# Performance work log

Measured on AMD Instinct MI355X. Metric: run time of the kernel, lower is better.

## Reference

```python
import jax, jax.numpy as jnp
import numpy as np

NUM_LEAVES = 8192
N_LAMBDA = 2101  # wavelengths 400..2500 nm

# ---- exponential integral E1(x), x > 0 (Abramowitz & Stegun 5.1.53 / 5.1.56) ----
# Ei(-x) = -E1(x) for x > 0; forward only ever calls expi on -kall with kall >= 1e-4.
_A = jnp.array([-0.57721566, 0.99999193, -0.24991055, 0.05519968, -0.00976004, 0.00107857], dtype=jnp.float32)
_PN = jnp.array([1.0, 8.5733287401, 18.0590169730, 8.6347608925, 0.2677737343], dtype=jnp.float32)
_PD = jnp.array([1.0, 9.5733223454, 25.6329561486, 21.0996530827, 3.9584969228], dtype=jnp.float32)

def _poly(c, x):
    r = c[0]
    for ci in c[1:]:
        r = r * x + ci
    return r

def _e1(x):
    # x > 0 guaranteed (kall clamped to >= 1e-4)
    small = -jnp.log(x) + _poly(_A[::-1], x)          # 0 < x <= 1
    big = jnp.exp(-x) / x * (_poly(_PN, x) / _poly(_PD, x))  # x > 1
    return jnp.where(x <= 1.0, small, big)

# ---- transmissivity of a dielectric plane (Stern / Allen) ----
def _getav(alpha_deg, nr):
    n2 = nr ** 2
    npx = n2 + 1.0
    nm = n2 - 1.0
    a = (nr + 1.0) * (nr + 1.0) / 2.0
    k = -(n2 - 1.0) * (n2 - 1.0) / 4.0
    rd = alpha_deg * (np.pi / 180.0)
    sa2 = np.sin(rd) ** 2  # python scalar
    if alpha_deg != 90.0:
        b1 = jnp.sqrt((sa2 - npx / 2.0) ** 2 + k)
    else:
        b1 = 0.0
    b2 = sa2 - npx / 2.0
    b = b1 - b2
    k2 = k ** 2
    ts = k2 / (6.0 * b ** 3) + k / b - b / 2.0 - (k2 / (6.0 * a ** 3) + k / a - a / 2.0)
    tp1 = -2.0 * n2 * (b - a) / npx ** 2
    nm2 = nm ** 2
    tp2 = -2.0 * n2 * npx * jnp.log(b / a) / nm2
    tp3 = n2 * (1.0 / b - 1.0 / a) / 2.0
    n22 = n2 ** 2
    npx3 = npx ** 3
    npax_a = 2.0 * npx * a - nm2
    npx_b = 2.0 * npx * b - nm2
    tp4 = 16.0 * n22 * (n22 + 1.0) * jnp.log(npx_b / npax_a) / (npx3 * nm2)
    tp5 = 16.0 * n2 ** 3 * (1.0 / npx_b - 1.0 / npax_a) / npx3
    tp = tp1 + tp2 + tp3 + tp4 + tp5
    return (ts + tp) / (2.0 * sa2)

def _forward(N, cab, car, water, lma, cant, nr, kab, kcar, kant, kw, km):
    # kall: [L, W] via broadcasting of [L,1] traits against [W] spectra
    kall = (cab * kab + car * kcar + cant * kant + water * kw + lma * km) / N
    kall = jnp.maximum(kall, 1e-4)
    # tau = (1-k)e^{-k} + k^2 * (-Ei(-k)) = (1-k)e^{-k} + k^2 E1(k)
    tau = (1.0 - kall) * jnp.exp(-kall) + kall ** 2 * _e1(kall)

    # one-layer reflectance/transmittance
    talf = _getav(40.0, nr)
    ralf = 1.0 - talf
    t12 = _getav(90.0, nr)
    r12 = 1.0 - t12
    t21 = t12 / (nr * nr)
    r21 = 1.0 - t21
    denom = 1.0 - r21 * r21 * tau * tau
    Ta = talf * tau * t21 / denom
    Ra = ralf + r21 * tau * Ta
    t = t12 * tau * t21 / denom
    r = r12 + r21 * tau * t

    rpt = r + t
    rmt = r - t
    mask = rpt >= 1.0  # [L, W]
    Dsq = (1.0 + rpt) * (1.0 + rmt) * (1.0 - rmt) * (1.0 - rpt)
    D = jnp.sqrt(jnp.where(mask, 1.0, Dsq))
    rqmtq = r ** 2 - t ** 2
    a = (1.0 + rqmtq + D) / (2.0 * r)
    b = (1.0 - rqmtq + D) / (2.0 * t)
    b_safe = jnp.where(mask, 1.0, b)  # guard pow with float exponent
    bnm1 = b_safe ** (N - 1.0)
    bn2 = bnm1 ** 2
    a2 = a * a
    den2 = a2 * bn2 - 1.0
    Rsub = a * (bn2 - 1.0) / den2
    Tsub = bnm1 * (a2 - 1.0) / den2
    # thick-layer (r+t >= 1) limit
    Tsub_alt = t / (t + (1.0 - t) * (N - 1.0))
    Tsub = jnp.where(mask, Tsub_alt, Tsub)
    Rsub = jnp.where(mask, 1.0 - Tsub_alt, Rsub)

    den3 = 1.0 - Rsub * r
    tran = Ta * Tsub / den3
    refl = Ra + Ta_Rsub_term(Ta, Rsub, t, den3)
    return refl, tran

def Ta_Rsub_term(Ta, Rsub, t, den3):
    return Ta * Rsub * t / den3

def setup_inputs() -> dict:
    key = jax.random.key(0)
    ks = jax.random.split(key, 12)
    u = lambda k, shp: jax.random.uniform(k, shp, dtype=jnp.float32)
    L, W = NUM_LEAVES, N_LAMBDA
    return {
        "N":     1.0 + 1.5 * u(ks[0], (L, 1)),      # leaf structure 1..2.5
        "cab":   10.0 + 70.0 * u(ks[1], (L, 1)),    # chlorophyll ug/cm2
        "car":   2.0 + 18.0 * u(ks[2], (L, 1)),     # carotenoids
        "water": 0.002 + 0.03 * u(ks[3], (L, 1)),   # EWT cm
        "lma":   0.005 + 0.03 * u(ks[4], (L, 1)),   # dry matter g/cm2
        "cant":  2.0 * u(ks[5], (L, 1)),            # anthocyanins
        "nr":    1.3 + 0.3 * u(ks[6], (W,)),        # refractive index
        "kab":   0.05 * u(ks[7], (W,)),
        "kcar":  0.05 * u(ks[8], (W,)),
        "kant":  0.05 * u(ks[9], (W,)),
        "kw":    30.0 * u(ks[10], (W,)),
        "km":    60.0 * u(ks[11], (W,)),
    }

def reference(N, cab, car, water, lma, cant, nr, kab, kcar, kant, kw, km):
    return _forward(N, cab, car, water, lma, cant, nr, kab, kcar, kant, kw, km)
```

## Files before the change

kernel.cpp:

```cpp
#include <hip/hip_runtime.h>

#define L_LEAVES 8192
#define W_LAMBDA 2101
#define WPAD     2104
#define NL       8
#define SA2_40   0.41317591116653485f
#define LOG2E_F  1.4426950408889634f
#define LN2_F    0.6931471805599453f

__device__ __forceinline__ float rcpf(float x)  { return __builtin_amdgcn_rcpf(x); }
__device__ __forceinline__ float log2f_fast(float x) { return __builtin_amdgcn_logf(x); }
__device__ __forceinline__ float exp2f_fast(float x) { return __builtin_amdgcn_exp2f(x); }
__device__ __forceinline__ float sqrtf_fast(float x) { return __builtin_amdgcn_sqrtf(x); }

__device__ __forceinline__ float getav_dev(float sa2, bool is90, float nr) {
    float n2  = nr * nr;
    float npx = n2 + 1.0f;
    float nm  = n2 - 1.0f;
    float a   = (nr + 1.0f) * (nr + 1.0f) * 0.5f;
    float k   = -(n2 - 1.0f) * (n2 - 1.0f) * 0.25f;
    float b2  = sa2 - npx * 0.5f;
    float b1  = is90 ? 0.0f : sqrtf(b2 * b2 + k);
    float b   = b1 - b2;
    float k2  = k * k;
    float b3  = b * b * b;
    float a3  = a * a * a;
    float ts  = k2 / (6.0f * b3) + k / b - b * 0.5f
              - (k2 / (6.0f * a3) + k / a - a * 0.5f);
    float tp1 = -2.0f * n2 * (b - a) / (npx * npx);
    float nm2 = nm * nm;
    float tp2 = -2.0f * n2 * npx * logf(b / a) / nm2;
    float tp3 = n2 * (1.0f / b - 1.0f / a) * 0.5f;
    float n22 = n2 * n2;
    float npx3 = npx * npx * npx;
    float npax_a = 2.0f * npx * a - nm2;
    float npx_b  = 2.0f * npx * b - nm2;
    float tp4 = 16.0f * n22 * (n22 + 1.0f) * logf(npx_b / npax_a) / (npx3 * nm2);
    float tp5 = 16.0f * n2 * n2 * n2 * (1.0f / npx_b - 1.0f / npax_a) / npx3;
    float tp  = tp1 + tp2 + tp3 + tp4 + tp5;
    return (ts + tp) / (2.0f * sa2);
}

__global__ void precompute_kernel(const float* __restrict__ nr, float* __restrict__ tab) {
    int w = blockIdx.x * blockDim.x + threadIdx.x;
    if (w >= W_LAMBDA) return;
    float n    = nr[w];
    float talf = getav_dev(SA2_40, false, n);
    float t12  = getav_dev(1.0f,   true,  n);
    float t21  = t12 * rcpf(n * n);
    float r21  = 1.0f - t21;
    tab[0 * WPAD + w] = talf * t21;
    tab[1 * WPAD + w] = 1.0f - talf;
    tab[2 * WPAD + w] = t12 * t21;
    tab[3 * WPAD + w] = 1.0f - t12;
    tab[4 * WPAD + w] = r21;
    tab[5 * WPAD + w] = r21 * r21;
}

struct f4u { float v[4]; };

__device__ __forceinline__ float vget(const float4& v, int j) {
    return j == 0 ? v.x : (j == 1 ? v.y : (j == 2 ? v.z : v.w));
}

template<bool USE_TAB>
__global__ __launch_bounds__(64) void prospect_kernel(
    const float* __restrict__ pN,   const float* __restrict__ pcab,
    const float* __restrict__ pcar, const float* __restrict__ pwater,
    const float* __restrict__ plma, const float* __restrict__ pcant,
    const float* __restrict__ pnr,
    const float* __restrict__ pkab, const float* __restrict__ pkcar,
    const float* __restrict__ pkant, const float* __restrict__ pkw,
    const float* __restrict__ pkm,
    const float* __restrict__ tab,
    float* __restrict__ out)
{
    const int q  = blockIdx.x * 64 + threadIdx.x;
    const int w0 = q * 4;
    if (w0 >= W_LAMBDA) return;
    const bool full = (w0 + 4 <= W_LAMBDA);
    const int l0 = blockIdx.y * NL;
    const size_t LW = (size_t)L_LEAVES * W_LAMBDA;

    float4 vkab, vkcar, vkant, vkw, vkm;
    float4 t0, t1, t2, t3, t4, t5;
    if (full) {
        vkab  = *(const float4*)(pkab  + w0);
        vkcar = *(const float4*)(pkcar + w0);
        vkant = *(const float4*)(pkant + w0);
        vkw   = *(const float4*)(pkw   + w0);
        vkm   = *(const float4*)(pkm   + w0);
    } else {
        #pragma unroll
        for (int j = 0; j < 4; ++j) {
            int w = min(w0 + j, W_LAMBDA - 1);
            ((float*)&vkab)[j]  = pkab[w];
            ((float*)&vkcar)[j] = pkcar[w];
            ((float*)&vkant)[j] = pkant[w];
            ((float*)&vkw)[j]   = pkw[w];
            ((float*)&vkm)[j]   = pkm[w];
        }
    }
    if (USE_TAB) {
        if (full) {
            t0 = *(const float4*)(tab + 0 * WPAD + w0);
            t1 = *(const float4*)(tab + 1 * WPAD + w0);
            t2 = *(const float4*)(tab + 2 * WPAD + w0);
            t3 = *(const float4*)(tab + 3 * WPAD + w0);
            t4 = *(const float4*)(tab + 4 * WPAD + w0);
            t5 = *(const float4*)(tab + 5 * WPAD + w0);
        } else {
            #pragma unroll
            for (int j = 0; j < 4; ++j) {
                int w = min(w0 + j, W_LAMBDA - 1);
                ((float*)&t0)[j] = tab[0 * WPAD + w];
                ((float*)&t1)[j] = tab[1 * WPAD + w];
                ((float*)&t2)[j] = tab[2 * WPAD + w];
                ((float*)&t3)[j] = tab[3 * WPAD + w];
                ((float*)&t4)[j] = tab[4 * WPAD + w];
                ((float*)&t5)[j] = tab[5 * WPAD + w];
            }
        }
    } else {
        #pragma unroll
        for (int j = 0; j < 4; ++j) {
            int w = min(w0 + j, W_LAMBDA - 1);
            float n    = pnr[w];
            float talf = getav_dev(SA2_40, false, n);
            float t12  = getav_dev(1.0f,   true,  n);
            float t21  = t12 * rcpf(n * n);
            float r21  = 1.0f - t21;
            ((float*)&t0)[j] = talf * t21;
            ((float*)&t1)[j] = 1.0f - talf;
            ((float*)&t2)[j] = t12 * t21;
            ((float*)&t3)[j] = 1.0f - t12;
            ((float*)&t4)[j] = r21;
            ((float*)&t5)[j] = r21 * r21;
        }
    }

    #pragma unroll 1
    for (int il = 0; il < NL; ++il) {
        const int l = l0 + il;
        const float Nl   = pN[l];
        const float invN = rcpf(Nl);
        const float Nm1  = Nl - 1.0f;
        const float cabl = pcab[l], carl = pcar[l], cantl = pcant[l];
        const float watl = pwater[l], lmal = plma[l];

        float rf[4], tr[4];
        #pragma unroll
        for (int j = 0; j < 4; ++j) {
            const float c0 = vget(t0, j), c1 = vget(t1, j), c2 = vget(t2, j);
            const float c3 = vget(t3, j), c4 = vget(t4, j), c5 = vget(t5, j);

            float k = (cabl * vget(vkab, j) + carl * vget(vkcar, j) + cantl * vget(vkant, j)
                     + watl * vget(vkw, j) + lmal * vget(vkm, j)) * invN;
            k = fmaxf(k, 1e-4f);

            float ek   = exp2f_fast(-k * LOG2E_F);
            float lg2k = log2f_fast(k);
            float poly = fmaf(fmaf(fmaf(fmaf(fmaf(0.00107857f, k, -0.00976004f), k, 0.05519968f),
                            k, -0.24991055f), k, 0.99999193f), k, -0.57721566f);
            float e1s  = fmaf(-LN2_F, lg2k, poly);
            float taus = fmaf(k * k, e1s, (1.0f - k) * ek);
            float pn = fmaf(fmaf(fmaf(fmaf(1.0f, k, 8.5733287401f), k, 18.0590169730f),
                           k, 8.6347608925f), k, 0.2677737343f);
            float pd = fmaf(fmaf(fmaf(fmaf(1.0f, k, 9.5733223454f), k, 25.6329561486f),
                           k, 21.0996530827f), k, 3.9584969228f);
            float taub = ek * fmaf(k, pn - pd, pd) * rcpf(pd);
            float tau  = (k <= 1.0f) ? taus : taub;

            float tau2 = tau * tau;
            float rd   = rcpf(fmaf(-c5, tau2, 1.0f));
            float Ta   = c0 * tau * rd;
            float tt   = c2 * tau * rd;
            float r21t = c4 * tau;
            float Ra   = fmaf(r21t, Ta, c1);
            float rr   = fmaf(r21t, tt, c3);

            float rpt  = rr + tt;
            float rmt  = rr - tt;
            bool  mask = (rpt >= 1.0f);
            float Dsq  = fmaf(-rmt, rmt, 1.0f) * fmaf(-rpt, rpt, 1.0f);
            float D    = sqrtf_fast(mask ? 1.0f : Dsq);
            float rq   = rpt * rmt;
            float s1   = 1.0f + D;
            float rp2  = rcpf((rr * tt) * 4.0f);
            float aa   = (s1 + rq) * (rp2 * (tt + tt));
            float bb   = (s1 - rq) * (rp2 * (rr + rr));
            float bsafe = mask ? 1.0f : bb;
            float bnm1 = exp2f_fast(Nm1 * log2f_fast(bsafe));
            float bn2  = bnm1 * bnm1;
            float a2   = aa * aa;
            float rdn  = rcpf(fmaf(a2, bn2, -1.0f));
            float Rsub = aa * (bn2 - 1.0f) * rdn;
            float Tsub = bnm1 * (a2 - 1.0f) * rdn;
            if (__any((int)mask)) {
                float Talt = tt * rcpf(fmaf(Nm1, 1.0f - tt, tt));
                if (mask) { Tsub = Talt; Rsub = 1.0f - Talt; }
            }

            float r3   = rcpf(fmaf(-Rsub, rr, 1.0f));
            float g    = Ta * r3;
            tr[j] = g * Tsub;
            rf[j] = fmaf(g * Rsub, tt, Ra);
        }

        const size_t base = (size_t)l * W_LAMBDA + w0;
        if (full) {
            f4u fr; f4u ft;
            #pragma unroll
            for (int j = 0; j < 4; ++j) { fr.v[j] = rf[j]; ft.v[j] = tr[j]; }
            *reinterpret_cast<f4u*>(out + base)      = fr;
            *reinterpret_cast<f4u*>(out + LW + base) = ft;
        } else {
            out[base]      = rf[0];
            out[LW + base] = tr[0];
        }
    }
}

extern "C" void kernel_launch(void* const* d_in, const int* in_sizes, int n_in,
                              void* d_out, int out_size, void* d_ws, size_t ws_size,
                              hipStream_t stream) {
    const float* pN     = (const float*)d_in[0];
    const float* pcab   = (const float*)d_in[1];
    const float* pcar   = (const float*)d_in[2];
    const float* pwater = (const float*)d_in[3];
    const float* plma   = (const float*)d_in[4];
    const float* pcant  = (const float*)d_in[5];
    const float* pnr    = (const float*)d_in[6];
    const float* pkab   = (const float*)d_in[7];
    const float* pkcar  = (const float*)d_in[8];
    const float* pkant  = (const float*)d_in[9];
    const float* pkw    = (const float*)d_in[10];
    const float* pkm    = (const float*)d_in[11];
    float* out = (float*)d_out;

    const int nquads = (W_LAMBDA + 3) / 4;
    dim3 grid((nquads + 63) / 64, L_LEAVES / NL);
    dim3 block(64);

    const size_t tab_bytes = 6 * WPAD * sizeof(float);
    if (ws_size >= tab_bytes) {
        float* tabp = (float*)d_ws;
        precompute_kernel<<<(W_LAMBDA + 255) / 256, 256, 0, stream>>>(pnr, tabp);
        prospect_kernel<true><<<grid, block, 0, stream>>>(
            pN, pcab, pcar, pwater, plma, pcant, pnr,
            pkab, pkcar, pkant, pkw, pkm, (const float*)tabp, out);
    } else {
        prospect_kernel<false><<<grid, block, 0, stream>>>(
            pN, pcab, pcar, pwater, plma, pcant, pnr,
            pkab, pkcar, pkant, pkw, pkm, nullptr, out);
    }
}
```

Baseline: 64.09 us.

## Assign one leaf per block row and merge substrate division algebra

Drops the per-thread loop over 8 leaves, so each block now handles a single leaf with 192 threads across wavelengths, and the grid grows to 8192 rows. The substrate and top-layer combination is rewritten algebraically so a single reciprocal replaces two. The aim is more parallelism and latency hiding, plus fewer transcendental ops per element. In exchange every thread reloads the per-wavelength spectra and table values for each leaf instead of reusing them across 8 leaves, which adds load traffic and many more blocks. It also wastes threads in the last column of blocks (526 quads spread over 3 blocks of 192).

```diff
diff --git a/kernel.cpp b/kernel.cpp
--- a/kernel.cpp
+++ b/kernel.cpp
@@ -3,7 +3,6 @@
 #define L_LEAVES 8192
 #define W_LAMBDA 2101
 #define WPAD     2104
-#define NL       8
 #define SA2_40   0.41317591116653485f
 #define LOG2E_F  1.4426950408889634f
 #define LN2_F    0.6931471805599453f
@@ -64,7 +63,7 @@
 }
 
 template<bool USE_TAB>
-__global__ __launch_bounds__(64) void prospect_kernel(
+__global__ __launch_bounds__(192) void prospect_kernel(
     const float* __restrict__ pN,   const float* __restrict__ pcab,
     const float* __restrict__ pcar, const float* __restrict__ pwater,
     const float* __restrict__ plma, const float* __restrict__ pcant,
@@ -75,11 +74,17 @@
     const float* __restrict__ tab,
     float* __restrict__ out)
 {
-    const int q  = blockIdx.x * 64 + threadIdx.x;
+    const int q  = blockIdx.x * blockDim.x + threadIdx.x;
     const int w0 = q * 4;
     if (w0 >= W_LAMBDA) return;
     const bool full = (w0 + 4 <= W_LAMBDA);
-    const int l0 = blockIdx.y * NL;
+
+    const int l = blockIdx.y;
+    const float Nl   = pN[l];
+    const float invN = rcpf(Nl);
+    const float Nm1  = Nl - 1.0f;
+    const float cabl = pcab[l], carl = pcar[l], cantl = pcant[l];
+    const float watl = pwater[l], lmal = plma[l];
     const size_t LW = (size_t)L_LEAVES * W_LAMBDA;
 
     float4 vkab, vkcar, vkant, vkw, vkm;
@@ -139,85 +144,82 @@
         }
     }
 
-    #pragma unroll 1
-    for (int il = 0; il < NL; ++il) {
-        const int l = l0 + il;
-        const float Nl   = pN[l];
-        const float invN = rcpf(Nl);
-        const float Nm1  = Nl - 1.0f;
-        const float cabl = pcab[l], carl = pcar[l], cantl = pcant[l];
-        const float watl = pwater[l], lmal = plma[l];
-
-        float rf[4], tr[4];
+    float rf[4], tr[4];
+    #pragma unroll
+    for (int j = 0; j < 4; ++j) {
+        const float c0 = vget(t0, j), c1 = vget(t1, j), c2 = vget(t2, j);
+        const float c3 = vget(t3, j), c4 = vget(t4, j), c5 = vget(t5, j);
+
+        float k = (cabl * vget(vkab, j) + carl * vget(vkcar, j) + cantl * vget(vkant, j)
+                 + watl * vget(vkw, j) + lmal * vget(vkm, j)) * invN;
+        k = fmaxf(k, 1e-4f);
+
+        float ek   = exp2f_fast(-k * LOG2E_F);
+        float lg2k = log2f_fast(k);
+        float poly = fmaf(fmaf(fmaf(fmaf(fmaf(0.00107857f, k, -0.00976004f), k, 0.05519968f),
+                        k, -0.24991055f), k, 0.99999193f), k, -0.57721566f);
+        float e1s  = fmaf(-LN2_F, lg2k, poly);
+        float taus = fmaf(k * k, e1s, fmaf(-k, ek, ek));
+        float pn = fmaf(fmaf(fmaf(k + 8.5733287401f, k, 18.0590169730f),
+                       k, 8.6347608925f), k, 0.2677737343f);
+        float pd = fmaf(fmaf(fmaf(k + 9.5733223454f, k, 25.6329561486f),
+                       k, 21.0996530827f), k, 3.9584969228f);
+        float taub = ek * fmaf(k, pn - pd, pd) * rcpf(pd);
+        float tau  = (k <= 1.0f) ? taus : taub;
+
+        float tau2 = tau * tau;
+        float rd   = rcpf(fmaf(-c5, tau2, 1.0f));
+        float trd  = tau * rd;
+        float Ta   = c0 * trd;
+        float tt   = c2 * trd;
+        float r21t = c4 * tau;
+        float Ra   = fmaf(r21t, Ta, c1);
+        float rr   = fmaf(r21t, tt, c3);
+
+        float rpt  = rr + tt;
+        float rmt  = rr - tt;
+        bool  mask = (rpt >= 1.0f);
+        float Dsq  = fmaf(-rmt, rmt, 1.0f) * fmaf(-rpt, rpt, 1.0f);
+        float D    = sqrtf_fast(mask ? 1.0f : Dsq);
+        float rq   = rpt * rmt;
+        float s1   = 1.0f + D;
+        float rp2  = rcpf((rr * tt) * 4.0f);
+        float aa   = (s1 + rq) * (rp2 * (tt + tt));
+        float bb   = (s1 - rq) * (rp2 * (rr + rr));
+        float bsafe = mask ? 1.0f : bb;
+        float bnm1 = exp2f_fast(Nm1 * log2f_fast(bsafe));
+        float bn2  = bnm1 * bnm1;
+        float a2   = aa * aa;
+        float den2 = fmaf(a2, bn2, -1.0f);
+        float bn2m1 = bn2 - 1.0f;
+        float aarr  = aa * rr;
+        float M     = fmaf(-aarr, bn2m1, den2);
+        float invM  = rcpf(M);
+        float TaM   = Ta * invM;
+        float tranj = TaM * bnm1 * (a2 - 1.0f);
+        float reflj = fmaf(TaM * tt * aa, bn2m1, Ra);
+
+        if (__any((int)mask)) {
+            float Talt = tt * rcpf(fmaf(Nm1, 1.0f - tt, tt));
+            float Rsm  = 1.0f - Talt;
+            float g    = Ta * rcpf(fmaf(-Rsm, rr, 1.0f));
+            if (mask) { tranj = g * Talt; reflj = fmaf(g * Rsm, tt, Ra); }
+        }
+
+        tr[j] = tranj;
+        rf[j] = reflj;
+    }
+
+    const size_t base = (size_t)l * W_LAMBDA + w0;
+    if (full) {
+        f4u fr; f4u ft;
         #pragma unroll
-        for (int j = 0; j < 4; ++j) {
-            const float c0 = vget(t0, j), c1 = vget(t1, j), c2 = vget(t2, j);
-            const float c3 = vget(t3, j), c4 = vget(t4, j), c5 = vget(t5, j);
-
-            float k = (cabl * vget(vkab, j) + carl * vget(vkcar, j) + cantl * vget(vkant, j)
-                     + watl * vget(vkw, j) + lmal * vget(vkm, j)) * invN;
-            k = fmaxf(k, 1e-4f);
-
-            float ek   = exp2f_fast(-k * LOG2E_F);
-            float lg2k = log2f_fast(k);
-            float poly = fmaf(fmaf(fmaf(fmaf(fmaf(0.00107857f, k, -0.00976004f), k, 0.05519968f),
-                            k, -0.24991055f), k, 0.99999193f), k, -0.57721566f);
-            float e1s  = fmaf(-LN2_F, lg2k, poly);
-            float taus = fmaf(k * k, e1s, (1.0f - k) * ek);
-            float pn = fmaf(fmaf(fmaf(fmaf(1.0f, k, 8.5733287401f), k, 18.0590169730f),
-                           k, 8.6347608925f), k, 0.2677737343f);
-            float pd = fmaf(fmaf(fmaf(fmaf(1.0f, k, 9.5733223454f), k, 25.6329561486f),
-                           k, 21.0996530827f), k, 3.9584969228f);
-            float taub = ek * fmaf(k, pn - pd, pd) * rcpf(pd);
-            float tau  = (k <= 1.0f) ? taus : taub;
-
-            float tau2 = tau * tau;
-            float rd   = rcpf(fmaf(-c5, tau2, 1.0f));
-            float Ta   = c0 * tau * rd;
-            float tt   = c2 * tau * rd;
-            float r21t = c4 * tau;
-            float Ra   = fmaf(r21t, Ta, c1);
-            float rr   = fmaf(r21t, tt, c3);
-
-            float rpt  = rr + tt;
-            float rmt  = rr - tt;
-            bool  mask = (rpt >= 1.0f);
-            float Dsq  = fmaf(-rmt, rmt, 1.0f) * fmaf(-rpt, rpt, 1.0f);
-            float D    = sqrtf_fast(mask ? 1.0f : Dsq);
-            float rq   = rpt * rmt;
-            float s1   = 1.0f + D;
-            float rp2  = rcpf((rr * tt) * 4.0f);
-            float aa   = (s1 + rq) * (rp2 * (tt + tt));
-            float bb   = (s1 - rq) * (rp2 * (rr + rr));
-            float bsafe = mask ? 1.0f : bb;
-            float bnm1 = exp2f_fast(Nm1 * log2f_fast(bsafe));
-            float bn2  = bnm1 * bnm1;
-            float a2   = aa * aa;
-            float rdn  = rcpf(fmaf(a2, bn2, -1.0f));
-            float Rsub = aa * (bn2 - 1.0f) * rdn;
-            float Tsub = bnm1 * (a2 - 1.0f) * rdn;
-            if (__any((int)mask)) {
-                float Talt = tt * rcpf(fmaf(Nm1, 1.0f - tt, tt));
-                if (mask) { Tsub = Talt; Rsub = 1.0f - Talt; }
-            }
-
-            float r3   = rcpf(fmaf(-Rsub, rr, 1.0f));
-            float g    = Ta * r3;
-            tr[j] = g * Tsub;
-            rf[j] = fmaf(g * Rsub, tt, Ra);
-        }
-
-        const size_t base = (size_t)l * W_LAMBDA + w0;
-        if (full) {
-            f4u fr; f4u ft;
-            #pragma unroll
-            for (int j = 0; j < 4; ++j) { fr.v[j] = rf[j]; ft.v[j] = tr[j]; }
-            *reinterpret_cast<f4u*>(out + base)      = fr;
-            *reinterpret_cast<f4u*>(out + LW + base) = ft;
-        } else {
-            out[base]      = rf[0];
-            out[LW + base] = tr[0];
-        }
+        for (int j = 0; j < 4; ++j) { fr.v[j] = rf[j]; ft.v[j] = tr[j]; }
+        *reinterpret_cast<f4u*>(out + base)      = fr;
+        *reinterpret_cast<f4u*>(out + LW + base) = ft;
+    } else {
+        out[base]      = rf[0];
+        out[LW + base] = tr[0];
     }
 }
 
@@ -239,8 +241,8 @@
     float* out = (float*)d_out;
 
     const int nquads = (W_LAMBDA + 3) / 4;
-    dim3 grid((nquads + 63) / 64, L_LEAVES / NL);
-    dim3 block(64);
+    dim3 grid((nquads + 191) / 192, L_LEAVES);
+    dim3 block(192);
 
     const size_t tab_bytes = 6 * WPAD * sizeof(float);
     if (ws_size >= tab_bytes) {
```

After: 60.03 us. -6.3%, faster.
